# Kernel optimization log

Measured on AMD Instinct MI355X. Metric: run time of the kernel, lower is better.

Reference implementation:

```python
import jax, jax.numpy as jnp
import numpy as np

B, T, D, H = 32, 256, 1024, 1024


def _flip_sequences(x, lengths):
    # Flip only the valid (unpadded) prefix of each sequence, as in flax sst2 util.
    max_len = x.shape[1]
    idxs = (jnp.arange(max_len - 1, -1, -1)[None, :] + lengths[:, None]) % max_len
    return x[jnp.arange(x.shape[0])[:, None], idxs]


def _lstm(x, Wi, Wh, b):
    # OptimizedLSTMCell math: z = x@Wi + h@Wh + b; gates (i, f, g, o);
    # c' = sig(f)*c + sig(i)*tanh(g); h' = sig(o)*tanh(c')
    batch = x.shape[0]
    hid = Wh.shape[0]
    xg = jnp.einsum('btd,dk->btk', x, Wi) + b  # precompute input projections [B,T,4H]

    def step(carry, xg_t):
        c, h = carry
        z = xg_t + h @ Wh
        i, f, g, o = jnp.split(z, 4, axis=-1)
        c = jax.nn.sigmoid(f) * c + jax.nn.sigmoid(i) * jnp.tanh(g)
        h = jax.nn.sigmoid(o) * jnp.tanh(c)
        return (c, h), h

    init = (jnp.zeros((batch, hid), x.dtype), jnp.zeros((batch, hid), x.dtype))
    _, hs = jax.lax.scan(step, init, jnp.swapaxes(xg, 0, 1))  # scan over time
    return jnp.swapaxes(hs, 0, 1)  # [B,T,H]


def setup_inputs() -> dict:
    key = jax.random.key(0)
    ks = jax.random.split(key, 7)
    si = 1.0 / np.sqrt(D)
    sh = 1.0 / np.sqrt(H)
    x = jax.random.normal(ks[0], (B, T, D), dtype=jnp.float32)
    mask = jnp.ones((B, T), dtype=jnp.int32)
    Wi_f = jax.random.normal(ks[1], (D, 4 * H), jnp.float32) * si
    Wh_f = jax.random.normal(ks[2], (H, 4 * H), jnp.float32) * sh
    b_f = jnp.zeros((4 * H,), jnp.float32)
    Wi_b = jax.random.normal(ks[3], (D, 4 * H), jnp.float32) * si
    Wh_b = jax.random.normal(ks[4], (H, 4 * H), jnp.float32) * sh
    b_b = jnp.zeros((4 * H,), jnp.float32)
    return {"x": x, "mask": mask, "Wi_f": Wi_f, "Wh_f": Wh_f, "b_f": b_f,
            "Wi_b": Wi_b, "Wh_b": Wh_b, "b_b": b_b}


def reference(x, mask, Wi_f, Wh_f, b_f, Wi_b, Wh_b, b_b):
    lengths = jnp.sum(mask, axis=1)
    fwd = _lstm(x, Wi_f, Wh_f, b_f)
    x_rev = _flip_sequences(x, lengths)
    bwd = _lstm(x_rev, Wi_b, Wh_b, b_b)
    bwd = _flip_sequences(bwd, lengths)
    return jnp.concatenate([fwd, bwd], axis=-1)  # [B,T,2H]
```

## Files before the change

kernel.cpp:

```cpp
#include <hip/hip_runtime.h>
#include <hip/hip_bf16.h>
#include <stdint.h>

typedef __attribute__((ext_vector_type(4))) float f32x4;
typedef __attribute__((ext_vector_type(8))) short short8;
typedef __attribute__((ext_vector_type(4))) short short4v;

#define OFF_XBF  ((size_t)0)
#define OFF_WIT  ((size_t)16777216)
#define OFF_WHT  ((size_t)33554432)
#define OFF_XG   ((size_t)50331648)
#define OFF_H    ((size_t)184549376)
#define OFF_BIAS ((size_t)184811520)
#define OFF_LEN  ((size_t)184844288)
#define OFF_CNT  ((size_t)184844416)

__device__ __forceinline__ short f2bf(float f) {
  union { float f; uint32_t u; } v; v.f = f;
  uint32_t u = v.u;
  uint32_t r = (u + 0x7fffu + ((u >> 16) & 1u)) >> 16;
  return (short)r;
}
__device__ __forceinline__ float bf2f(short s) {
  union { uint32_t u; float f; } v; v.u = ((uint32_t)(uint16_t)s) << 16;
  return v.f;
}
__device__ __forceinline__ float sigf(float z) {
  float e = __builtin_amdgcn_exp2f(z * -1.44269504f);
  return __builtin_amdgcn_rcpf(1.f + e);
}
__device__ __forceinline__ float tanhfast(float z) {
  float e = __builtin_amdgcn_exp2f(z * -2.88539008f);
  return fmaf(__builtin_amdgcn_rcpf(1.f + e), 2.f, -1.f);
}

__global__ void k_len(const int* __restrict__ mask, int* __restrict__ len) {
  int b = threadIdx.x;
  if (b < 32) {
    int s = 0;
    for (int t = 0; t < 256; t++) s += mask[b * 256 + t];
    len[b] = s;
  }
}

__global__ void k_xconv(const float* __restrict__ x, short* __restrict__ xbf) {
  int bid = blockIdx.x;
  int b = bid >> 8, t = bid & 255;
  int d = threadIdx.x * 4;
  const float* sp = x + ((size_t)bid) * 1024 + d;
  float4 v = *(const float4*)sp;
  short4v o;
  o.x = f2bf(v.x); o.y = f2bf(v.y); o.z = f2bf(v.z); o.w = f2bf(v.w);
  *(short4v*)(xbf + ((size_t)(t * 32 + b)) * 1024 + d) = o;
}

__global__ void k_wprep(const float* __restrict__ Wi_f, const float* __restrict__ Wi_b,
                        const float* __restrict__ Wh_f, const float* __restrict__ Wh_b,
                        short* __restrict__ WiT, short* __restrict__ WhT) {
  __shared__ short ldsT[64 * 72];
  int id = blockIdx.x;
  int which = id >> 11, dir = (id >> 10) & 1, tile = id & 1023;
  int kt = (tile >> 6) * 64, c0 = (tile & 63) * 64;
  const float* src = (which == 0) ? (dir == 0 ? Wi_f : Wi_b)
                                  : (dir == 0 ? Wh_f : Wh_b);
  short* dst = (which == 0) ? WiT : WhT;
  int tid = threadIdx.x;
#pragma unroll 4
  for (int i = 0; i < 16; i++) {
    int idx = i * 256 + tid;
    int kk = idx >> 6, cc = idx & 63;
    float v = src[(size_t)(kt + kk) * 4096 + c0 + cc];
    ldsT[cc * 72 + kk] = f2bf(v);
  }
  __syncthreads();
  int rowc = tid >> 2, part = tid & 3;
  int cg = c0 + rowc;
  int gate = cg >> 10, hc = cg & 1023;
  int p = (hc >> 2) * 16 + gate * 4 + (hc & 3);
  int n = dir * 4096 + p;
  short8 v0 = *(short8*)&ldsT[rowc * 72 + part * 16];
  short8 v1 = *(short8*)&ldsT[rowc * 72 + part * 16 + 8];
  *(short8*)(dst + (size_t)n * 1024 + kt + part * 16) = v0;
  *(short8*)(dst + (size_t)n * 1024 + kt + part * 16 + 8) = v1;
}

__global__ void k_bias(const float* __restrict__ bf_, const float* __restrict__ bb_,
                       float* __restrict__ bp) {
  int n = blockIdx.x * 256 + threadIdx.x;
  int dir = n >> 12, p = n & 4095;
  int gate = (p >> 2) & 3, g4 = p >> 4, h4 = p & 3;
  int c = gate * 1024 + g4 * 4 + h4;
  bp[n] = (dir == 0 ? bf_ : bb_)[c];
}

__global__ void k_gemm(const short* __restrict__ Abf,
                       const short* __restrict__ Bbf,
                       const float* __restrict__ bias,
                       short* __restrict__ C) {
  __shared__ char Ash[128 * 144];
  __shared__ char Bsh[128 * 144];
  const int tid = threadIdx.x;
  const int lane = tid & 63, wid = tid >> 6;
  const int wm = wid >> 1, wn = wid & 1;
  const int l15 = lane & 15, lg = lane >> 4;
  const int m0 = blockIdx.y * 128, n0 = blockIdx.x * 128;

  f32x4 acc[4][4];
#pragma unroll
  for (int i = 0; i < 4; i++)
#pragma unroll
    for (int j = 0; j < 4; j++) acc[i][j] = (f32x4){0.f, 0.f, 0.f, 0.f};

  for (int kt = 0; kt < 1024; kt += 64) {
#pragma unroll
    for (int i = 0; i < 4; i++) {
      int chunk = i * 256 + tid;
      int row = chunk >> 3, kc = chunk & 7;
      *(short8*)(Ash + row * 144 + kc * 16) =
          *(const short8*)(Abf + (size_t)(m0 + row) * 1024 + kt + kc * 8);
      *(short8*)(Bsh + row * 144 + kc * 16) =
          *(const short8*)(Bbf + (size_t)(n0 + row) * 1024 + kt + kc * 8);
    }
    __syncthreads();
#pragma unroll
    for (int kk = 0; kk < 2; kk++) {
      short8 af[4], bfv[4];
#pragma unroll
      for (int mt = 0; mt < 4; mt++)
        af[mt] = *(const short8*)(Ash + (wm * 64 + mt * 16 + l15) * 144 + kk * 64 + lg * 16);
#pragma unroll
      for (int ntc = 0; ntc < 4; ntc++)
        bfv[ntc] = *(const short8*)(Bsh + (wn * 64 + ntc * 16 + l15) * 144 + kk * 64 + lg * 16);
#pragma unroll
      for (int mt = 0; mt < 4; mt++)
#pragma unroll
        for (int ntc = 0; ntc < 4; ntc++)
          acc[mt][ntc] = __builtin_amdgcn_mfma_f32_16x16x32_bf16(af[mt], bfv[ntc], acc[mt][ntc], 0, 0, 0);
    }
    __syncthreads();
  }
  float bs[4];
#pragma unroll
  for (int ntc = 0; ntc < 4; ntc++) bs[ntc] = bias[n0 + wn * 64 + ntc * 16 + l15];
#pragma unroll
  for (int mt = 0; mt < 4; mt++) {
    int row = m0 + wm * 64 + mt * 16 + lg * 4;
#pragma unroll
    for (int ntc = 0; ntc < 4; ntc++) {
      int col = n0 + wn * 64 + ntc * 16 + l15;
#pragma unroll
      for (int r = 0; r < 4; r++)
        C[(size_t)(row + r) * 8192 + col] = f2bf(acc[mt][ntc][r] + bs[ntc]);
    }
  }
}

__global__ void __launch_bounds__(512, 1) k_recur(
    const short* __restrict__ XG,
    const short* __restrict__ WhT,
    const int* __restrict__ len,
    short* __restrict__ hbuf,
    float* __restrict__ out,
    unsigned int* __restrict__ flags) {
  __shared__ char Hld[66560];
  char* Pub = Hld + 65536;
  char* hb = (char*)hbuf;
  const int tid = threadIdx.x;
  const int lane = tid & 63;
  const int wid = tid >> 6;
  const int bidx = blockIdx.x;
  const int dir = bidx >> 6;
  const int nblk = bidx & 63;
  const int mt = wid >> 2, nt = wid & 3;
  const int l15 = lane & 15, lg = lane >> 4;

  const int ncol = dir * 4096 + nblk * 64 + nt * 16 + l15;
  const short* wrow = WhT + (size_t)ncol * 1024;
  short8 bfr[32];
#pragma unroll
  for (int kk = 0; kk < 32; kk++)
    bfr[kk] = *(const short8*)(wrow + kk * 32 + lg * 8);

  float c_reg[4] = {0.f, 0.f, 0.f, 0.f};
  int lenv[4];
#pragma unroll
  for (int r = 0; r < 4; r++) lenv[r] = len[mt * 16 + lg * 4 + r];

  const int c4 = l15;
  const int gate = c4 >> 2;
  const int brow = mt * 16 + l15;
  const int sw = (brow & 7) << 4;
  const int abase = brow * 2048 + (lg << 4);
  const int hcol0 = nblk * 16 + nt * 4;
  unsigned int* dflags = flags + dir * 64;

  float xg_pf[4];
#pragma unroll
  for (int r = 0; r < 4; r++) {
    int b_r = mt * 16 + lg * 4 + r;
    int tt = (dir == 0) ? 0 : ((lenv[r] - 1) & 255);
    xg_pf[r] = bf2f(XG[(size_t)(tt * 32 + b_r) * 8192 + ncol]);
  }

  const int myb = lane >> 1;
  const int mysw = (myb & 7) << 4;
  const int mybase = myb * 2048 + (lane & 1) * 16;

  for (int t = 0; t < 256; t++) {
    {
      const unsigned int* fl = dflags + wid * 8 + (lane & 7);
      unsigned int tgt = (unsigned int)t;
      for (;;) {
        unsigned int v = __hip_atomic_load(fl, __ATOMIC_RELAXED, __HIP_MEMORY_SCOPE_AGENT);
        if (__all((int)(v >= tgt))) break;
      }
      __builtin_amdgcn_sched_barrier(0);
      const char* hsrcB = hb + (size_t)(((t & 1) * 2 + dir) * 65536);
      f32x4 sv[8];
#pragma unroll
      for (int j = 0; j < 8; j++) {
        const char* a = hsrcB + (wid * 8 + j) * 1024 + lane * 16;
        asm volatile("global_load_dwordx4 %0, %1, off sc0 sc1" : "=v"(sv[j]) : "v"(a));
      }
      asm volatile("s_waitcnt vmcnt(0)" ::: "memory");
      __builtin_amdgcn_sched_barrier(0);
#pragma unroll
      for (int j = 0; j < 8; j++) {
        int off = (mybase + (wid * 8 + j) * 32) ^ mysw;
        *(f32x4*)(Hld + off) = sv[j];
      }
    }
    __syncthreads();

    f32x4 accA = (f32x4){0.f, 0.f, 0.f, 0.f};
    f32x4 accB = (f32x4){0.f, 0.f, 0.f, 0.f};
#pragma unroll
    for (int kk = 0; kk < 16; kk++) {
      short8 afA = *(const short8*)(Hld + ((abase + kk * 64) ^ sw));
      short8 afB = *(const short8*)(Hld + ((abase + (kk + 16) * 64) ^ sw));
      accA = __builtin_amdgcn_mfma_f32_16x16x32_bf16(afA, bfr[kk], accA, 0, 0, 0);
      accB = __builtin_amdgcn_mfma_f32_16x16x32_bf16(afB, bfr[kk + 16], accB, 0, 0, 0);
    }

    f32x4 hsave[4];
#pragma unroll
    for (int r = 0; r < 4; r++) {
      int b_r = mt * 16 + lg * 4 + r;
      float z = accA[r] + accB[r] + xg_pf[r];
      float s = (gate == 2) ? tanhfast(z) : sigf(z);
      float x8 = __shfl_xor(s, 8);
      float pI = s * x8;
      float v = (gate == 0) ? pI : s;
      float x4 = __shfl_xor(v, 4);
      float o4 = __shfl_xor(x8, 4);
      float cn = fmaf(x4, c_reg[r], pI);
      float h = o4 * tanhfast(cn);
      if (c4 < 4) c_reg[r] = cn;
      uint32_t hb16 = (uint32_t)(uint16_t)f2bf(h);
      uint32_t p0 = hb16 | (__shfl_xor(hb16, 1) << 16);
      uint32_t q  = __shfl_xor(p0, 2);
      if (c4 == 0) {
        unsigned long long p = (unsigned long long)p0 | ((unsigned long long)q << 32);
        *(unsigned long long*)(Pub + b_r * 32 + nt * 8) = p;
        hsave[r].x = bf2f((short)(p0 & 0xffff));
        hsave[r].y = bf2f((short)(p0 >> 16));
        hsave[r].z = bf2f((short)(q & 0xffff));
        hsave[r].w = bf2f((short)(q >> 16));
      }
    }
    __syncthreads();

    if (wid == 0) {
      f32x4 pv = *(const f32x4*)(Pub + lane * 16);
      char* hdstB = hb + (size_t)((((t + 1) & 1) * 2 + dir) * 65536) + nblk * 1024 + lane * 16;
      asm volatile("global_store_dwordx4 %0, %1, off sc0 sc1" :: "v"(hdstB), "v"(pv) : "memory");
      asm volatile("s_waitcnt vmcnt(0)" ::: "memory");
      if (lane == 0)
        __hip_atomic_store(dflags + nblk, (unsigned int)(t + 1),
                           __ATOMIC_RELAXED, __HIP_MEMORY_SCOPE_AGENT);
    }
    __builtin_amdgcn_sched_barrier(0);

    if (c4 == 0) {
#pragma unroll
      for (int r = 0; r < 4; r++) {
        int b_r = mt * 16 + lg * 4 + r;
        int tt = (dir == 0) ? t : ((lenv[r] - 1 - t) & 255);
        *(f32x4*)(out + ((size_t)b_r * 256 + tt) * 2048 + dir * 1024 + hcol0) = hsave[r];
      }
    }
    int tn = (t < 255) ? t + 1 : 255;
#pragma unroll
    for (int r = 0; r < 4; r++) {
      int b_r = mt * 16 + lg * 4 + r;
      int tt = (dir == 0) ? tn : ((lenv[r] - 1 - tn) & 255);
      xg_pf[r] = bf2f(XG[(size_t)(tt * 32 + b_r) * 8192 + ncol]);
    }
  }
}

extern "C" void kernel_launch(void* const* d_in, const int* in_sizes, int n_in,
                              void* d_out, int out_size, void* d_ws, size_t ws_size,
                              hipStream_t stream) {
  const float* x    = (const float*)d_in[0];
  const int*   mask = (const int*)d_in[1];
  const float* Wi_f = (const float*)d_in[2];
  const float* Wh_f = (const float*)d_in[3];
  const float* b_f  = (const float*)d_in[4];
  const float* Wi_b = (const float*)d_in[5];
  const float* Wh_b = (const float*)d_in[6];
  const float* b_b  = (const float*)d_in[7];
  float* out = (float*)d_out;
  char* ws = (char*)d_ws;

  short* xbf  = (short*)(ws + OFF_XBF);
  short* WiT  = (short*)(ws + OFF_WIT);
  short* WhT  = (short*)(ws + OFF_WHT);
  short* XG   = (short*)(ws + OFF_XG);
  short* hbuf = (short*)(ws + OFF_H);
  float* bp   = (float*)(ws + OFF_BIAS);
  int*   len  = (int*)(ws + OFF_LEN);
  unsigned int* flags = (unsigned int*)(ws + OFF_CNT);

  hipMemsetAsync(hbuf, 0, 262144, stream);
  hipMemsetAsync(flags, 0, 512, stream);

  k_len<<<1, 64, 0, stream>>>(mask, len);
  k_xconv<<<8192, 256, 0, stream>>>(x, xbf);
  k_wprep<<<4096, 256, 0, stream>>>(Wi_f, Wi_b, Wh_f, Wh_b, WiT, WhT);
  k_bias<<<32, 256, 0, stream>>>(b_f, b_b, bp);

  dim3 g(64, 64);
  k_gemm<<<g, 256, 0, stream>>>(xbf, WiT, bp, XG);

  k_recur<<<128, 512, 0, stream>>>(XG, WhT, len, hbuf, out, flags);
}
```

Measured before the change: 1.365 ms.

## Replace flag-based step sync with per-word timestep tags embedded in hidden-state buffer

Each bf16 hidden value is stored together with a 16-bit timestep tag in a 32-bit word. Consumers poll the data itself and reload only the chunks whose tags do not match, instead of spinning on separate flags before loading the data. This removes the store-wait-then-flag round trip and the serialized flag poll from every recurrent step. The cost is twice the bytes of hidden-state traffic, tag packing and unpacking work, and reuse of the dead WiT workspace region for the tag buffer, which is cleared after the GEMM.

```diff
diff --git a/kernel.cpp b/kernel.cpp
--- a/kernel.cpp
+++ b/kernel.cpp
@@ -5,15 +5,14 @@
 typedef __attribute__((ext_vector_type(4))) float f32x4;
 typedef __attribute__((ext_vector_type(8))) short short8;
 typedef __attribute__((ext_vector_type(4))) short short4v;
+typedef __attribute__((ext_vector_type(4))) int int4v;
 
 #define OFF_XBF  ((size_t)0)
 #define OFF_WIT  ((size_t)16777216)
 #define OFF_WHT  ((size_t)33554432)
 #define OFF_XG   ((size_t)50331648)
-#define OFF_H    ((size_t)184549376)
 #define OFF_BIAS ((size_t)184811520)
 #define OFF_LEN  ((size_t)184844288)
-#define OFF_CNT  ((size_t)184844416)
 
 __device__ __forceinline__ short f2bf(float f) {
   union { float f; uint32_t u; } v; v.f = f;
@@ -159,12 +158,11 @@
     const short* __restrict__ XG,
     const short* __restrict__ WhT,
     const int* __restrict__ len,
-    short* __restrict__ hbuf,
-    float* __restrict__ out,
-    unsigned int* __restrict__ flags) {
+    unsigned int* __restrict__ htag,
+    float* __restrict__ out) {
   __shared__ char Hld[66560];
   char* Pub = Hld + 65536;
-  char* hb = (char*)hbuf;
+  char* tb_base = (char*)htag;
   const int tid = threadIdx.x;
   const int lane = tid & 63;
   const int wid = tid >> 6;
@@ -192,7 +190,6 @@
   const int sw = (brow & 7) << 4;
   const int abase = brow * 2048 + (lg << 4);
   const int hcol0 = nblk * 16 + nt * 4;
-  unsigned int* dflags = flags + dir * 64;
 
   float xg_pf[4];
 #pragma unroll
@@ -205,29 +202,54 @@
   const int myb = lane >> 1;
   const int mysw = (myb & 7) << 4;
   const int mybase = myb * 2048 + (lane & 1) * 16;
+  const int srcoff = myb * 64 + (lane & 1) * 32;
 
   for (int t = 0; t < 256; t++) {
+    const char* tb  = tb_base + (size_t)((t & 1) * 2 + dir) * 131072;
+    char* tbn       = tb_base + (size_t)(((t + 1) & 1) * 2 + dir) * 131072;
+    const uint32_t exp = (uint32_t)t;
+
     {
-      const unsigned int* fl = dflags + wid * 8 + (lane & 7);
-      unsigned int tgt = (unsigned int)t;
-      for (;;) {
-        unsigned int v = __hip_atomic_load(fl, __ATOMIC_RELAXED, __HIP_MEMORY_SCOPE_AGENT);
-        if (__all((int)(v >= tgt))) break;
-      }
-      __builtin_amdgcn_sched_barrier(0);
-      const char* hsrcB = hb + (size_t)(((t & 1) * 2 + dir) * 65536);
-      f32x4 sv[8];
+      int4v v[8][2];
+      const char* a0 = tb + srcoff;
 #pragma unroll
       for (int j = 0; j < 8; j++) {
-        const char* a = hsrcB + (wid * 8 + j) * 1024 + lane * 16;
-        asm volatile("global_load_dwordx4 %0, %1, off sc0 sc1" : "=v"(sv[j]) : "v"(a));
+        const char* a = a0 + (wid * 8 + j) * 2048;
+        asm volatile("global_load_dwordx4 %0, %1, off sc0 sc1" : "=v"(v[j][0]) : "v"(a));
+        asm volatile("global_load_dwordx4 %0, %1, off sc0 sc1" : "=v"(v[j][1]) : "v"(a + 16));
       }
       asm volatile("s_waitcnt vmcnt(0)" ::: "memory");
       __builtin_amdgcn_sched_barrier(0);
+      for (;;) {
+        uint32_t bad = 0;
+#pragma unroll
+        for (int j = 0; j < 8; j++) {
+          uint32_t m = (((uint32_t)v[j][0].x ^ exp) | ((uint32_t)v[j][0].y ^ exp) |
+                        ((uint32_t)v[j][0].z ^ exp) | ((uint32_t)v[j][0].w ^ exp) |
+                        ((uint32_t)v[j][1].x ^ exp) | ((uint32_t)v[j][1].y ^ exp) |
+                        ((uint32_t)v[j][1].z ^ exp) | ((uint32_t)v[j][1].w ^ exp)) & 0xffffu;
+          if (m) bad |= 1u << j;
+        }
+        if (!bad) break;
+#pragma unroll
+        for (int j = 0; j < 8; j++)
+          if (bad & (1u << j)) {
+            const char* a = a0 + (wid * 8 + j) * 2048;
+            asm volatile("global_load_dwordx4 %0, %1, off sc0 sc1" : "=v"(v[j][0]) : "v"(a));
+            asm volatile("global_load_dwordx4 %0, %1, off sc0 sc1" : "=v"(v[j][1]) : "v"(a + 16));
+          }
+        asm volatile("s_waitcnt vmcnt(0)" ::: "memory");
+        __builtin_amdgcn_sched_barrier(0);
+      }
 #pragma unroll
       for (int j = 0; j < 8; j++) {
+        int4v w;
+        w.x = (int)((((uint32_t)v[j][0].x) >> 16) | (((uint32_t)v[j][0].y) & 0xffff0000u));
+        w.y = (int)((((uint32_t)v[j][0].z) >> 16) | (((uint32_t)v[j][0].w) & 0xffff0000u));
+        w.z = (int)((((uint32_t)v[j][1].x) >> 16) | (((uint32_t)v[j][1].y) & 0xffff0000u));
+        w.w = (int)((((uint32_t)v[j][1].z) >> 16) | (((uint32_t)v[j][1].w) & 0xffff0000u));
         int off = (mybase + (wid * 8 + j) * 32) ^ mysw;
-        *(f32x4*)(Hld + off) = sv[j];
+        *(int4v*)(Hld + off) = w;
       }
     }
     __syncthreads();
@@ -271,13 +293,20 @@
     __syncthreads();
 
     if (wid == 0) {
-      f32x4 pv = *(const f32x4*)(Pub + lane * 16);
-      char* hdstB = hb + (size_t)((((t + 1) & 1) * 2 + dir) * 65536) + nblk * 1024 + lane * 16;
-      asm volatile("global_store_dwordx4 %0, %1, off sc0 sc1" :: "v"(hdstB), "v"(pv) : "memory");
-      asm volatile("s_waitcnt vmcnt(0)" ::: "memory");
-      if (lane == 0)
-        __hip_atomic_store(dflags + nblk, (unsigned int)(t + 1),
-                           __ATOMIC_RELAXED, __HIP_MEMORY_SCOPE_AGENT);
+      int4v pv = *(const int4v*)(Pub + lane * 16);
+      uint32_t tg = (uint32_t)(t + 1);
+      int4v e0, e1;
+      e0.x = (int)((((uint32_t)pv.x) << 16) | tg);
+      e0.y = (int)((((uint32_t)pv.x) & 0xffff0000u) | tg);
+      e0.z = (int)((((uint32_t)pv.y) << 16) | tg);
+      e0.w = (int)((((uint32_t)pv.y) & 0xffff0000u) | tg);
+      e1.x = (int)((((uint32_t)pv.z) << 16) | tg);
+      e1.y = (int)((((uint32_t)pv.z) & 0xffff0000u) | tg);
+      e1.z = (int)((((uint32_t)pv.w) << 16) | tg);
+      e1.w = (int)((((uint32_t)pv.w) & 0xffff0000u) | tg);
+      char* d0 = tbn + nblk * 2048 + (lane >> 1) * 64 + (lane & 1) * 32;
+      asm volatile("global_store_dwordx4 %0, %1, off sc0 sc1" :: "v"(d0), "v"(e0) : "memory");
+      asm volatile("global_store_dwordx4 %0, %1, off sc0 sc1" :: "v"(d0 + 16), "v"(e1) : "memory");
     }
     __builtin_amdgcn_sched_barrier(0);
 
@@ -317,13 +346,9 @@
   short* WiT  = (short*)(ws + OFF_WIT);
   short* WhT  = (short*)(ws + OFF_WHT);
   short* XG   = (short*)(ws + OFF_XG);
-  short* hbuf = (short*)(ws + OFF_H);
   float* bp   = (float*)(ws + OFF_BIAS);
   int*   len  = (int*)(ws + OFF_LEN);
-  unsigned int* flags = (unsigned int*)(ws + OFF_CNT);
-
-  hipMemsetAsync(hbuf, 0, 262144, stream);
-  hipMemsetAsync(flags, 0, 512, stream);
+  unsigned int* htag = (unsigned int*)(ws + OFF_WIT);
 
   k_len<<<1, 64, 0, stream>>>(mask, len);
   k_xconv<<<8192, 256, 0, stream>>>(x, xbf);
@@ -333,5 +358,7 @@
   dim3 g(64, 64);
   k_gemm<<<g, 256, 0, stream>>>(xbf, WiT, bp, XG);
 
-  k_recur<<<128, 512, 0, stream>>>(XG, WhT, len, hbuf, out, flags);
-}
+  hipMemsetAsync(htag, 0, 524288, stream);
+
+  k_recur<<<128, 512, 0, stream>>>(XG, WhT, len, htag, out);
+}
```

Result: slower. 3.587 ms (+162.7%).

## Halve recurrent kernel blocks; each wave handles both batch tiles

Applied to the files above, without the earlier changes.

The persistent LSTM recurrence kernel now runs on 64 blocks instead of 128. Each wave covers 16 gate columns across both 16-row batch tiles rather than one tile, so a block owns 128 gate columns. This halves the number of blocks that must publish and poll flags at every timestep, which is meant to cut grid-wide synchronisation and global h-exchange overhead. In exchange each wave does twice the MFMA and gate work per step, and only 64 CUs are used.

```diff
diff --git a/kernel.cpp b/kernel.cpp
--- a/kernel.cpp
+++ b/kernel.cpp
@@ -162,118 +162,126 @@
     short* __restrict__ hbuf,
     float* __restrict__ out,
     unsigned int* __restrict__ flags) {
-  __shared__ char Hld[66560];
+  __shared__ char Hld[67584];
   char* Pub = Hld + 65536;
   char* hb = (char*)hbuf;
   const int tid = threadIdx.x;
   const int lane = tid & 63;
   const int wid = tid >> 6;
   const int bidx = blockIdx.x;
-  const int dir = bidx >> 6;
-  const int nblk = bidx & 63;
-  const int mt = wid >> 2, nt = wid & 3;
+  const int dir = bidx >> 5;
+  const int nblk = bidx & 31;
+  const int nt = wid;
   const int l15 = lane & 15, lg = lane >> 4;
 
-  const int ncol = dir * 4096 + nblk * 64 + nt * 16 + l15;
+  const int ncol = dir * 4096 + nblk * 128 + nt * 16 + l15;
   const short* wrow = WhT + (size_t)ncol * 1024;
   short8 bfr[32];
 #pragma unroll
   for (int kk = 0; kk < 32; kk++)
     bfr[kk] = *(const short8*)(wrow + kk * 32 + lg * 8);
 
-  float c_reg[4] = {0.f, 0.f, 0.f, 0.f};
-  int lenv[4];
-#pragma unroll
-  for (int r = 0; r < 4; r++) lenv[r] = len[mt * 16 + lg * 4 + r];
+  float c_reg[2][4] = {{0.f,0.f,0.f,0.f},{0.f,0.f,0.f,0.f}};
+  int lenv[2][4];
+  float xg_pf[2][4];
+#pragma unroll
+  for (int mt = 0; mt < 2; mt++)
+#pragma unroll
+    for (int r = 0; r < 4; r++) {
+      int b_r = mt * 16 + lg * 4 + r;
+      lenv[mt][r] = len[b_r];
+      int tt = (dir == 0) ? 0 : ((lenv[mt][r] - 1) & 255);
+      xg_pf[mt][r] = bf2f(XG[(size_t)(tt * 32 + b_r) * 8192 + ncol]);
+    }
 
   const int c4 = l15;
   const int gate = c4 >> 2;
-  const int brow = mt * 16 + l15;
-  const int sw = (brow & 7) << 4;
-  const int abase = brow * 2048 + (lg << 4);
-  const int hcol0 = nblk * 16 + nt * 4;
-  unsigned int* dflags = flags + dir * 64;
-
-  float xg_pf[4];
-#pragma unroll
-  for (int r = 0; r < 4; r++) {
-    int b_r = mt * 16 + lg * 4 + r;
-    int tt = (dir == 0) ? 0 : ((lenv[r] - 1) & 255);
-    xg_pf[r] = bf2f(XG[(size_t)(tt * 32 + b_r) * 8192 + ncol]);
-  }
-
-  const int myb = lane >> 1;
-  const int mysw = (myb & 7) << 4;
-  const int mybase = myb * 2048 + (lane & 1) * 16;
+  const int sw = (l15 & 7) << 4;
+  const int hcol0 = nblk * 32 + nt * 4;
+  unsigned int* dflags = flags + dir * 32;
+
+  const int srow = lane & 31;
+  const int shalf = lane >> 5;
+  const int mysw = (srow & 7) << 4;
 
   for (int t = 0; t < 256; t++) {
+    const char* tb = hb + (size_t)((t & 1) * 2 + dir) * 65536;
+    char* tbn      = hb + (size_t)(((t + 1) & 1) * 2 + dir) * 65536;
+
     {
-      const unsigned int* fl = dflags + wid * 8 + (lane & 7);
+      const unsigned int* fl = dflags + wid * 4 + (lane & 3);
       unsigned int tgt = (unsigned int)t;
       for (;;) {
         unsigned int v = __hip_atomic_load(fl, __ATOMIC_RELAXED, __HIP_MEMORY_SCOPE_AGENT);
         if (__all((int)(v >= tgt))) break;
       }
       __builtin_amdgcn_sched_barrier(0);
-      const char* hsrcB = hb + (size_t)(((t & 1) * 2 + dir) * 65536);
-      f32x4 sv[8];
-#pragma unroll
-      for (int j = 0; j < 8; j++) {
-        const char* a = hsrcB + (wid * 8 + j) * 1024 + lane * 16;
-        asm volatile("global_load_dwordx4 %0, %1, off sc0 sc1" : "=v"(sv[j]) : "v"(a));
+      f32x4 sv[4][2];
+#pragma unroll
+      for (int p = 0; p < 4; p++) {
+        const char* a = tb + (wid * 4 + p) * 2048 + srow * 64 + shalf * 32;
+        asm volatile("global_load_dwordx4 %0, %1, off sc0 sc1" : "=v"(sv[p][0]) : "v"(a));
+        asm volatile("global_load_dwordx4 %0, %1, off sc0 sc1" : "=v"(sv[p][1]) : "v"(a + 16));
       }
       asm volatile("s_waitcnt vmcnt(0)" ::: "memory");
       __builtin_amdgcn_sched_barrier(0);
 #pragma unroll
-      for (int j = 0; j < 8; j++) {
-        int off = (mybase + (wid * 8 + j) * 32) ^ mysw;
-        *(f32x4*)(Hld + off) = sv[j];
+      for (int p = 0; p < 4; p++) {
+        int off = srow * 2048 + (wid * 4 + p) * 64 + shalf * 32;
+        *(f32x4*)(Hld + (off ^ mysw)) = sv[p][0];
+        *(f32x4*)(Hld + ((off + 16) ^ mysw)) = sv[p][1];
       }
     }
     __syncthreads();
 
-    f32x4 accA = (f32x4){0.f, 0.f, 0.f, 0.f};
-    f32x4 accB = (f32x4){0.f, 0.f, 0.f, 0.f};
-#pragma unroll
-    for (int kk = 0; kk < 16; kk++) {
-      short8 afA = *(const short8*)(Hld + ((abase + kk * 64) ^ sw));
-      short8 afB = *(const short8*)(Hld + ((abase + (kk + 16) * 64) ^ sw));
-      accA = __builtin_amdgcn_mfma_f32_16x16x32_bf16(afA, bfr[kk], accA, 0, 0, 0);
-      accB = __builtin_amdgcn_mfma_f32_16x16x32_bf16(afB, bfr[kk + 16], accB, 0, 0, 0);
-    }
-
-    f32x4 hsave[4];
-#pragma unroll
-    for (int r = 0; r < 4; r++) {
-      int b_r = mt * 16 + lg * 4 + r;
-      float z = accA[r] + accB[r] + xg_pf[r];
-      float s = (gate == 2) ? tanhfast(z) : sigf(z);
-      float x8 = __shfl_xor(s, 8);
-      float pI = s * x8;
-      float v = (gate == 0) ? pI : s;
-      float x4 = __shfl_xor(v, 4);
-      float o4 = __shfl_xor(x8, 4);
-      float cn = fmaf(x4, c_reg[r], pI);
-      float h = o4 * tanhfast(cn);
-      if (c4 < 4) c_reg[r] = cn;
-      uint32_t hb16 = (uint32_t)(uint16_t)f2bf(h);
-      uint32_t p0 = hb16 | (__shfl_xor(hb16, 1) << 16);
-      uint32_t q  = __shfl_xor(p0, 2);
-      if (c4 == 0) {
-        unsigned long long p = (unsigned long long)p0 | ((unsigned long long)q << 32);
-        *(unsigned long long*)(Pub + b_r * 32 + nt * 8) = p;
-        hsave[r].x = bf2f((short)(p0 & 0xffff));
-        hsave[r].y = bf2f((short)(p0 >> 16));
-        hsave[r].z = bf2f((short)(q & 0xffff));
-        hsave[r].w = bf2f((short)(q >> 16));
-      }
-    }
+    f32x4 acc[2][2];
+#pragma unroll
+    for (int mt = 0; mt < 2; mt++) {
+      acc[mt][0] = (f32x4){0.f, 0.f, 0.f, 0.f};
+      acc[mt][1] = (f32x4){0.f, 0.f, 0.f, 0.f};
+      const int ab = (mt * 16 + l15) * 2048 + (lg << 4);
+#pragma unroll
+      for (int kk = 0; kk < 16; kk++) {
+        short8 afA = *(const short8*)(Hld + ((ab + kk * 64) ^ sw));
+        short8 afB = *(const short8*)(Hld + ((ab + (kk + 16) * 64) ^ sw));
+        acc[mt][0] = __builtin_amdgcn_mfma_f32_16x16x32_bf16(afA, bfr[kk], acc[mt][0], 0, 0, 0);
+        acc[mt][1] = __builtin_amdgcn_mfma_f32_16x16x32_bf16(afB, bfr[kk + 16], acc[mt][1], 0, 0, 0);
+      }
+    }
+
+    uint32_t hsv0[2][4], hsv1[2][4];
+#pragma unroll
+    for (int mt = 0; mt < 2; mt++)
+#pragma unroll
+      for (int r = 0; r < 4; r++) {
+        int b_r = mt * 16 + lg * 4 + r;
+        float z = acc[mt][0][r] + acc[mt][1][r] + xg_pf[mt][r];
+        float s = (gate == 2) ? tanhfast(z) : sigf(z);
+        float x8 = __shfl_xor(s, 8);
+        float pI = s * x8;
+        float v = (gate == 0) ? pI : s;
+        float x4 = __shfl_xor(v, 4);
+        float o4 = __shfl_xor(x8, 4);
+        float cn = fmaf(x4, c_reg[mt][r], pI);
+        float h = o4 * tanhfast(cn);
+        if (c4 < 4) c_reg[mt][r] = cn;
+        uint32_t hb16 = (uint32_t)(uint16_t)f2bf(h);
+        uint32_t p0 = hb16 | (__shfl_xor(hb16, 1) << 16);
+        uint32_t q  = __shfl_xor(p0, 2);
+        hsv0[mt][r] = p0; hsv1[mt][r] = q;
+        if (c4 == 0) {
+          unsigned long long p = (unsigned long long)p0 | ((unsigned long long)q << 32);
+          *(unsigned long long*)(Pub + b_r * 64 + nt * 8) = p;
+        }
+      }
     __syncthreads();
 
     if (wid == 0) {
-      f32x4 pv = *(const f32x4*)(Pub + lane * 16);
-      char* hdstB = hb + (size_t)((((t + 1) & 1) * 2 + dir) * 65536) + nblk * 1024 + lane * 16;
-      asm volatile("global_store_dwordx4 %0, %1, off sc0 sc1" :: "v"(hdstB), "v"(pv) : "memory");
+      f32x4 pv0 = *(const f32x4*)(Pub + lane * 32);
+      f32x4 pv1 = *(const f32x4*)(Pub + lane * 32 + 16);
+      char* d = tbn + nblk * 2048 + lane * 32;
+      asm volatile("global_store_dwordx4 %0, %1, off sc0 sc1" :: "v"(d), "v"(pv0) : "memory");
+      asm volatile("global_store_dwordx4 %0, %1, off sc0 sc1" :: "v"(d + 16), "v"(pv1) : "memory");
       asm volatile("s_waitcnt vmcnt(0)" ::: "memory");
       if (lane == 0)
         __hip_atomic_store(dflags + nblk, (unsigned int)(t + 1),
@@ -283,19 +291,28 @@
 
     if (c4 == 0) {
 #pragma unroll
+      for (int mt = 0; mt < 2; mt++)
+#pragma unroll
+        for (int r = 0; r < 4; r++) {
+          int b_r = mt * 16 + lg * 4 + r;
+          int tt = (dir == 0) ? t : ((lenv[mt][r] - 1 - t) & 255);
+          f32x4 hv;
+          hv.x = bf2f((short)(hsv0[mt][r] & 0xffff));
+          hv.y = bf2f((short)(hsv0[mt][r] >> 16));
+          hv.z = bf2f((short)(hsv1[mt][r] & 0xffff));
+          hv.w = bf2f((short)(hsv1[mt][r] >> 16));
+          *(f32x4*)(out + ((size_t)b_r * 256 + tt) * 2048 + dir * 1024 + hcol0) = hv;
+        }
+    }
+    int tn = (t < 255) ? t + 1 : 255;
+#pragma unroll
+    for (int mt = 0; mt < 2; mt++)
+#pragma unroll
       for (int r = 0; r < 4; r++) {
         int b_r = mt * 16 + lg * 4 + r;
-        int tt = (dir == 0) ? t : ((lenv[r] - 1 - t) & 255);
-        *(f32x4*)(out + ((size_t)b_r * 256 + tt) * 2048 + dir * 1024 + hcol0) = hsave[r];
-      }
-    }
-    int tn = (t < 255) ? t + 1 : 255;
-#pragma unroll
-    for (int r = 0; r < 4; r++) {
-      int b_r = mt * 16 + lg * 4 + r;
-      int tt = (dir == 0) ? tn : ((lenv[r] - 1 - tn) & 255);
-      xg_pf[r] = bf2f(XG[(size_t)(tt * 32 + b_r) * 8192 + ncol]);
-    }
+        int tt = (dir == 0) ? tn : ((lenv[mt][r] - 1 - tn) & 255);
+        xg_pf[mt][r] = bf2f(XG[(size_t)(tt * 32 + b_r) * 8192 + ncol]);
+      }
   }
 }
 
@@ -333,5 +350,5 @@
   dim3 g(64, 64);
   k_gemm<<<g, 256, 0, stream>>>(xbf, WiT, bp, XG);
 
-  k_recur<<<128, 512, 0, stream>>>(XG, WhT, len, hbuf, out, flags);
-}
+  k_recur<<<64, 512, 0, stream>>>(XG, WhT, len, hbuf, out, flags);
+}
```

Measured after the change: 2.554 ms. 87.1% more time.
